# Kernel optimization log

Hardware: AMD Instinct MI355X
Metric: run time of the kernel (lower is better)

## Reference

```python
import jax, jax.numpy as jnp
import numpy as np

N = 131072   # batch of trajectory points
DX = 2       # state dim (module hardcodes Linear(2,300) in vv)
H_TM = 100   # taskmap coupling-layer hidden
H_VV = 300   # vv net hidden
H_VS = 100   # vel-scalar coupling-layer hidden


def setup_inputs() -> dict:
    key = jax.random.key(0)
    ks = iter(jax.random.split(key, 40))
    def W(i, o):
        return jax.random.normal(next(ks), (i, o), jnp.float32) / np.float32(np.sqrt(i))
    def b(o):
        return 0.01 * jax.random.normal(next(ks), (o,), jnp.float32)
    d = {"x": jax.random.normal(next(ks), (N, DX), jnp.float32)}
    # taskmap CouplingLayer nn1 (tanh MLP, residual)
    d.update(tm1_w1=W(DX, H_TM), tm1_b1=b(H_TM), tm1_w2=W(H_TM, H_TM), tm1_b2=b(H_TM), tm1_w3=W(H_TM, DX), tm1_b3=b(DX))
    # taskmap CouplingLayer nn2_1 (elu MLP -> softplus gate)
    d.update(tm2_w1=W(DX, H_TM), tm2_b1=b(H_TM), tm2_w2=W(H_TM, H_TM), tm2_b2=b(H_TM), tm2_w3=W(H_TM, DX), tm2_b3=b(DX))
    # vv net: Linear(2,300) PReLU Linear(300,300) PReLU Linear(300,2)
    d.update(vv_w1=W(DX, H_VV), vv_b1=b(H_VV), vv_a1=jnp.full((1,), 0.25, jnp.float32),
             vv_w2=W(H_VV, H_VV), vv_b2=b(H_VV), vv_a2=jnp.full((1,), 0.25, jnp.float32),
             vv_w3=W(H_VV, DX), vv_b3=b(DX))
    # log_vel_scalar CouplingLayer nn3 (leaky_relu MLP, residual via broadcast)
    d.update(vs_w1=W(DX, H_VS), vs_b1=b(H_VS), vs_w2=W(H_VS, H_VS), vs_b2=b(H_VS), vs_w3=W(H_VS, 1), vs_b3=b(1))
    return d


def reference(x, tm1_w1, tm1_b1, tm1_w2, tm1_b2, tm1_w3, tm1_b3,
              tm2_w1, tm2_b1, tm2_w2, tm2_b2, tm2_w3, tm2_b3,
              vv_w1, vv_b1, vv_a1, vv_w2, vv_b2, vv_a2, vv_w3, vv_b3,
              vs_w1, vs_b1, vs_w2, vs_b2, vs_w3, vs_b3):
    def taskmap(z):  # CouplingLayer forward with is_diffeomorphism=True; z (..., DX)
        h = jnp.tanh(z @ tm1_w1 + tm1_b1)
        h = jnp.tanh(h @ tm1_w2 + tm1_b2)
        y1 = h @ tm1_w3 + tm1_b3 + z
        g = jax.nn.elu(y1 @ tm2_w1 + tm2_b1)
        g = jax.nn.elu(g @ tm2_w2 + tm2_b2)
        s = jax.nn.softplus(g @ tm2_w3 + tm2_b3)
        return s * y1 + y1

    prelu = lambda t, a: jnp.where(t >= 0, t, a * t)
    leaky = lambda t: jnp.where(t >= 0, t, 0.01 * t)

    origin_y = taskmap(jnp.zeros((1, DX), x.dtype))        # taskmap_fcn(origin)
    y = taskmap(x) - origin_y                              # y_hat (N, DX)
    J = jax.vmap(jax.jacfwd(taskmap))(x)                   # J_hat (N, DX, DX)

    # doty_pre = vv(y_hat)
    h = prelu(y @ vv_w1 + vv_b1, vv_a1)
    h = prelu(h @ vv_w2 + vv_b2, vv_a2)
    doty = h @ vv_w3 + vv_b3                               # (N, DX)

    ls_var = jnp.sum(doty * y, axis=-1, keepdims=True)     # (N, 1)
    V_y = jnp.sum(y * y, axis=-1, keepdims=True)           # (N, 1)
    yd = doty - jax.nn.relu(ls_var + 1e-4 * V_y) * y / (V_y + 1e-12)

    J_inv = jnp.linalg.pinv(J)                             # batched pseudo-inverse
    yd_n = yd / jnp.maximum(jnp.linalg.norm(yd, axis=-1, keepdims=True), 1e-12)  # F.normalize
    xd_hat = jnp.einsum('nij,nj->ni', J_inv, yd_n)         # bmm then squeeze

    # vel_scalar = exp(log_vel_scalar(x)) + eps;  log_vel_scalar = nn3(x) + x  (broadcast (N,1)+(N,DX))
    hs = leaky(x @ vs_w1 + vs_b1)
    hs = leaky(hs @ vs_w2 + vs_b2)
    logv = (hs @ vs_w3 + vs_b3) + x                        # (N, DX) via broadcast
    xd = (jnp.exp(logv) + 1e-12) * xd_hat
    return xd
```

## Files before the change

### kernel.cpp

```cpp
#include <hip/hip_runtime.h>
#include <math.h>

#define H1 100
#define H3 300

#define WT_TM1    0
#define WT_TM2    14336
#define WT_VS     28672
#define WT_VV     43008
#define NSHORT    140288
#define F_TM1W1   0
#define F_TM1B1   256
#define F_TM2W1   384
#define F_TM2B1   640
#define F_VSW1    768
#define F_VSB1    1024
#define F_VVW1    1152
#define F_VVB1    1792
#define F_TM1B2   2112
#define F_TM2B2   2240
#define F_VSB2    2368
#define F_VVB2    2496
#define F_TM1W3T  2816
#define F_TM2W3T  3072
#define F_VSW3T   3328
#define F_VVW3T   3456
#define NFLOAT    4096

typedef __attribute__((ext_vector_type(8))) short s8v;
typedef __attribute__((ext_vector_type(4))) float f4v;

__device__ __forceinline__ f4v mfma16(s8v a, s8v b, f4v c) {
    return __builtin_amdgcn_mfma_f32_16x16x32_bf16(a, b, c, 0, 0, 0);
}
__device__ __forceinline__ float rcp_fast(float v) { return __builtin_amdgcn_rcpf(v); }
__device__ __forceinline__ float tanh_fast(float v) {
    float t = __expf(2.f * v);
    return 1.f - 2.f * rcp_fast(t + 1.f);
}
__device__ __forceinline__ float leakyf(float v) { return v >= 0.f ? v : 0.01f * v; }
__device__ __forceinline__ float preluf(float v, float a) { return v >= 0.f ? v : a * v; }
__device__ __forceinline__ short f2bf(float f) {
    union { float f; unsigned u; } v; v.f = f;
    unsigned r = v.u + 0x7fffu + ((v.u >> 16) & 1u);
    return (short)(r >> 16);
}
#define RED4(v) { v += __shfl_xor(v, 16, 64); v += __shfl_xor(v, 32, 64); }

__global__ void ngdv_prep(
    const float* __restrict__ tm1_w1, const float* __restrict__ tm1_b1,
    const float* __restrict__ tm1_w2, const float* __restrict__ tm1_b2,
    const float* __restrict__ tm1_w3, const float* __restrict__ tm1_b3,
    const float* __restrict__ tm2_w1, const float* __restrict__ tm2_b1,
    const float* __restrict__ tm2_w2, const float* __restrict__ tm2_b2,
    const float* __restrict__ tm2_w3, const float* __restrict__ tm2_b3,
    const float* __restrict__ vs_w1,  const float* __restrict__ vs_b1,
    const float* __restrict__ vs_w2,  const float* __restrict__ vs_b2,
    const float* __restrict__ vs_w3,
    const float* __restrict__ vv_w1,  const float* __restrict__ vv_b1,
    const float* __restrict__ vv_w2,  const float* __restrict__ vv_b2,
    const float* __restrict__ vv_w3,
    short* __restrict__ wsb, float* __restrict__ wsf, float* __restrict__ origin_out)
{
    const int tid = threadIdx.x;
    if (blockIdx.x < 564) {
        int idx = blockIdx.x * 256 + tid;
        if (idx < NSHORT) {
            short o;
            if (idx < WT_VV) {
                int rgn = idx / 14336, r = idx % 14336;
                const float* src = (rgn == 0) ? tm1_w2 : (rgn == 1) ? tm2_w2 : vs_w2;
                int nt = r >> 11, ks = (r >> 9) & 3, lane = (r >> 3) & 63, e = r & 7;
                int n = nt*16 + (lane & 15);
                int k = ks*32 + (lane >> 4)*8 + e;
                o = (n < H1 && k < H1) ? f2bf(src[k*H1 + n]) : (short)0;
            } else {
                int r = idx - WT_VV;
                int nt = r / 5120, rem = r % 5120;
                int ks = rem >> 9, lane = (rem >> 3) & 63, e = r & 7;
                int n = nt*16 + (lane & 15);
                int k = ks*32 + (lane >> 4)*8 + e;
                o = (n < H3 && k < H3) ? f2bf(vv_w2[k*H3 + n]) : (short)0;
            }
            wsb[idx] = o;
        } else {
            int f = idx - NSHORT;
            if (f < NFLOAT) {
                float v = 0.f;
                if (f < 256)       { int d = f >> 7, c = f & 127; if (c < H1) v = tm1_w1[d*H1 + c]; }
                else if (f < 384)  { int c = f - 256;  if (c < H1) v = tm1_b1[c]; }
                else if (f < 640)  { int r = f - 384, d = r >> 7, c = r & 127; if (c < H1) v = tm2_w1[d*H1 + c]; }
                else if (f < 768)  { int c = f - 640;  if (c < H1) v = tm2_b1[c]; }
                else if (f < 1024) { int r = f - 768, d = r >> 7, c = r & 127; if (c < H1) v = vs_w1[d*H1 + c]; }
                else if (f < 1152) { int c = f - 1024; if (c < H1) v = vs_b1[c]; }
                else if (f < 1792) { int r = f - 1152, d = r / 320, c = r % 320; if (c < H3) v = vv_w1[d*H3 + c]; }
                else if (f < 2112) { int c = f - 1792; if (c < H3) v = vv_b1[c]; }
                else if (f < 2240) { int c = f - 2112; if (c < H1) v = tm1_b2[c]; }
                else if (f < 2368) { int c = f - 2240; if (c < H1) v = tm2_b2[c]; }
                else if (f < 2496) { int c = f - 2368; if (c < H1) v = vs_b2[c]; }
                else if (f < 2816) { int c = f - 2496; if (c < H3) v = vv_b2[c]; }
                else if (f < 3072) { int r = f - 2816, i = r >> 7, c = r & 127; if (c < H1) v = tm1_w3[c*2 + i]; }
                else if (f < 3328) { int r = f - 3072, i = r >> 7, c = r & 127; if (c < H1) v = tm2_w3[c*2 + i]; }
                else if (f < 3456) { int c = f - 3328; if (c < H1) v = vs_w3[c]; }
                else               { int r = f - 3456, i = r / 320, c = r % 320; if (c < H3) v = vv_w3[c*2 + i]; }
                wsf[f] = v;
            }
        }
        return;
    }
    __shared__ float h1[H1], h2[H1], y1o[2], g1[H1], g2[H1];
    const int r = tid >> 1, hf = tid & 1;
    const int k0 = hf ? 50 : 0, k1 = hf ? 100 : 50;
    if (tid < H1) h1[tid] = tanhf(tm1_b1[tid]);
    __syncthreads();
    {
        float acc = 0.f;
        if (r < H1) for (int k = k0; k < k1; ++k) acc += h1[k] * tm1_w2[k*H1 + r];
        acc += __shfl_xor(acc, 1, 64);
        if (r < H1 && !hf) h2[r] = tanhf(acc + tm1_b2[r]);
    }
    __syncthreads();
    if (tid < 2) {
        float acc = tm1_b3[tid];
        for (int k = 0; k < H1; ++k) acc += h2[k] * tm1_w3[k*2 + tid];
        y1o[tid] = acc;
    }
    __syncthreads();
    if (tid < H1) {
        float pre = tm2_b1[tid] + y1o[0]*tm2_w1[tid] + y1o[1]*tm2_w1[H1 + tid];
        g1[tid] = pre > 0.f ? pre : expm1f(pre);
    }
    __syncthreads();
    {
        float acc = 0.f;
        if (r < H1) for (int k = k0; k < k1; ++k) acc += g1[k] * tm2_w2[k*H1 + r];
        acc += __shfl_xor(acc, 1, 64);
        if (r < H1 && !hf) { float a = acc + tm2_b2[r]; g2[r] = a > 0.f ? a : expm1f(a); }
    }
    __syncthreads();
    if (tid < 2) {
        float acc = tm2_b3[tid];
        for (int k = 0; k < H1; ++k) acc += g2[k] * tm2_w3[k*2 + tid];
        float s = acc > 20.f ? acc : log1pf(expf(acc));
        origin_out[tid] = (1.f + s) * y1o[tid];
    }
}

__global__ __launch_bounds__(512, 2) void ngdv_main(
    const float* __restrict__ x,
    const float* __restrict__ tm1_b3, const float* __restrict__ tm2_b3,
    const float* __restrict__ vs_b3,  const float* __restrict__ vv_b3,
    const float* __restrict__ vv_a1,  const float* __restrict__ vv_a2,
    const short* __restrict__ wsb,    const float* __restrict__ wsf,
    const float* __restrict__ origin, float* __restrict__ out, int npts)
{
    __shared__ __align__(16) float LW[4096];
    __shared__ __align__(16) short TMB[14336];
    __shared__ __align__(16) short VVB[2][20480];

    const int tid = threadIdx.x;
    const int wv = tid >> 6, lane = tid & 63;
    const int fm = lane & 15, fq = lane >> 4;
    const int p = blockIdx.x*128 + wv*16 + fm;
    float2 xv = {0.f, 0.f};
    if (p < npts) xv = *(const float2*)&x[p*2];
    const float og0 = origin[0], og1 = origin[1];

    for (int i = tid; i < 1024; i += 512) ((f4v*)LW)[i] = ((const f4v*)wsf)[i];
    {
        const s8v* s = (const s8v*)(wsb + WT_TM1);
        s8v* d = (s8v*)TMB;
        for (int i = tid; i < 1792; i += 512) d[i] = s[i];
    }
    __syncthreads();
    const float a1v = vv_a1[0], a2v = vv_a2[0];

    s8v afp[4], aft0[4], aft1[4];

    #pragma unroll
    for (int ks = 0; ks < 4; ++ks) {
        int c0 = ks*32 + fq*8;
        #pragma unroll
        for (int hh = 0; hh < 2; ++hh) {
            f4v w0 = *(const f4v*)&LW[F_TM1W1 + c0 + hh*4];
            f4v w1 = *(const f4v*)&LW[F_TM1W1 + 128 + c0 + hh*4];
            f4v bv = *(const f4v*)&LW[F_TM1B1 + c0 + hh*4];
            #pragma unroll
            for (int e = 0; e < 4; ++e) {
                int ee = hh*4 + e;
                float pre = fmaf(xv.y, w1[e], fmaf(xv.x, w0[e], bv[e]));
                float h = tanh_fast(pre), dd = 1.f - h*h;
                afp[ks][ee] = f2bf(h);
                aft0[ks][ee] = f2bf(w0[e]*dd);
                aft1[ks][ee] = f2bf(w1[e]*dd);
            }
        }
    }

    float y1p0 = 0.f, y1p1 = 0.f, dyp00 = 0.f, dyp01 = 0.f, dyp10 = 0.f, dyp11 = 0.f;
    #pragma unroll
    for (int nt = 0; nt < 7; ++nt) {
        s8v b0 = *(const s8v*)&TMB[(nt*4+0)*512 + lane*8];
        s8v b1 = *(const s8v*)&TMB[(nt*4+1)*512 + lane*8];
        s8v b2 = *(const s8v*)&TMB[(nt*4+2)*512 + lane*8];
        s8v b3 = *(const s8v*)&TMB[(nt*4+3)*512 + lane*8];
        f4v cp = {0,0,0,0}, ct0 = {0,0,0,0}, ct1 = {0,0,0,0};
        cp  = mfma16(b0, afp[0], cp);   cp  = mfma16(b1, afp[1], cp);
        cp  = mfma16(b2, afp[2], cp);   cp  = mfma16(b3, afp[3], cp);
        ct0 = mfma16(b0, aft0[0], ct0); ct0 = mfma16(b1, aft0[1], ct0);
        ct0 = mfma16(b2, aft0[2], ct0); ct0 = mfma16(b3, aft0[3], ct0);
        ct1 = mfma16(b0, aft1[0], ct1); ct1 = mfma16(b1, aft1[1], ct1);
        ct1 = mfma16(b2, aft1[2], ct1); ct1 = mfma16(b3, aft1[3], ct1);
        int col0 = nt*16 + fq*4;
        f4v bb2 = *(const f4v*)&LW[F_TM1B2 + col0];
        f4v w0v = *(const f4v*)&LW[F_TM1W3T + col0];
        f4v w1v = *(const f4v*)&LW[F_TM1W3T + 128 + col0];
        #pragma unroll
        for (int r = 0; r < 4; ++r) {
            float h = tanh_fast(cp[r] + bb2[r]);
            float dd = 1.f - h*h;
            float t0 = ct0[r]*dd, t1 = ct1[r]*dd;
            y1p0  = fmaf(h,  w0v[r], y1p0);  y1p1  = fmaf(h,  w1v[r], y1p1);
            dyp00 = fmaf(t0, w0v[r], dyp00); dyp01 = fmaf(t0, w1v[r], dyp01);
            dyp10 = fmaf(t1, w0v[r], dyp10); dyp11 = fmaf(t1, w1v[r], dyp11);
        }
    }
    RED4(y1p0); RED4(y1p1); RED4(dyp00); RED4(dyp01); RED4(dyp10); RED4(dyp11);
    const float y10 = y1p0 + tm1_b3[0] + xv.x;
    const float y11 = y1p1 + tm1_b3[1] + xv.y;
    const float dy00 = dyp00 + 1.f, dy01 = dyp01;
    const float dy10 = dyp10, dy11 = dyp11 + 1.f;
    __syncthreads();

    {
        const s8v* s = (const s8v*)(wsb + WT_TM2);
        s8v* d = (s8v*)TMB;
        for (int i = tid; i < 1792; i += 512) d[i] = s[i];
    }
    __syncthreads();

    #pragma unroll
    for (int ks = 0; ks < 4; ++ks) {
        int c0 = ks*32 + fq*8;
        #pragma unroll
        for (int hh = 0; hh < 2; ++hh) {
            f4v w0 = *(const f4v*)&LW[F_TM2W1 + c0 + hh*4];
            f4v w1 = *(const f4v*)&LW[F_TM2W1 + 128 + c0 + hh*4];
            f4v bv = *(const f4v*)&LW[F_TM2B1 + c0 + hh*4];
            #pragma unroll
            for (int e = 0; e < 4; ++e) {
                int ee = hh*4 + e;
                float pre = fmaf(y11, w1[e], fmaf(y10, w0[e], bv[e]));
                float g = pre > 0.f ? pre : (__expf(pre) - 1.f);
                float dd = pre > 0.f ? 1.f : (g + 1.f);
                afp[ks][ee] = f2bf(g);
                aft0[ks][ee] = f2bf((dy00*w0[e] + dy01*w1[e]) * dd);
                aft1[ks][ee] = f2bf((dy10*w0[e] + dy11*w1[e]) * dd);
            }
        }
    }

    float spp0 = 0.f, spp1 = 0.f, dsp00 = 0.f, dsp01 = 0.f, dsp10 = 0.f, dsp11 = 0.f;
    #pragma unroll
    for (int nt = 0; nt < 7; ++nt) {
        s8v b0 = *(const s8v*)&TMB[(nt*4+0)*512 + lane*8];
        s8v b1 = *(const s8v*)&TMB[(nt*4+1)*512 + lane*8];
        s8v b2 = *(const s8v*)&TMB[(nt*4+2)*512 + lane*8];
        s8v b3 = *(const s8v*)&TMB[(nt*4+3)*512 + lane*8];
        f4v cp = {0,0,0,0}, ct0 = {0,0,0,0}, ct1 = {0,0,0,0};
        cp  = mfma16(b0, afp[0], cp);   cp  = mfma16(b1, afp[1], cp);
        cp  = mfma16(b2, afp[2], cp);   cp  = mfma16(b3, afp[3], cp);
        ct0 = mfma16(b0, aft0[0], ct0); ct0 = mfma16(b1, aft0[1], ct0);
        ct0 = mfma16(b2, aft0[2], ct0); ct0 = mfma16(b3, aft0[3], ct0);
        ct1 = mfma16(b0, aft1[0], ct1); ct1 = mfma16(b1, aft1[1], ct1);
        ct1 = mfma16(b2, aft1[2], ct1); ct1 = mfma16(b3, aft1[3], ct1);
        int col0 = nt*16 + fq*4;
        f4v bb2 = *(const f4v*)&LW[F_TM2B2 + col0];
        f4v w0v = *(const f4v*)&LW[F_TM2W3T + col0];
        f4v w1v = *(const f4v*)&LW[F_TM2W3T + 128 + col0];
        #pragma unroll
        for (int r = 0; r < 4; ++r) {
            float pre = cp[r] + bb2[r];
            float g = pre > 0.f ? pre : (__expf(pre) - 1.f);
            float dd = pre > 0.f ? 1.f : (g + 1.f);
            float t0 = ct0[r]*dd, t1 = ct1[r]*dd;
            spp0  = fmaf(g,  w0v[r], spp0);  spp1  = fmaf(g,  w1v[r], spp1);
            dsp00 = fmaf(t0, w0v[r], dsp00); dsp01 = fmaf(t0, w1v[r], dsp01);
            dsp10 = fmaf(t1, w0v[r], dsp10); dsp11 = fmaf(t1, w1v[r], dsp11);
        }
    }
    RED4(spp0); RED4(spp1); RED4(dsp00); RED4(dsp01); RED4(dsp10); RED4(dsp11);
    float ys0, ys1, Ja, Jb, Jc, Jd;
    {
        float sp0 = spp0 + tm2_b3[0], sp1 = spp1 + tm2_b3[1];
        float s0 = sp0 > 20.f ? sp0 : __logf(1.f + __expf(sp0));
        float s1 = sp1 > 20.f ? sp1 : __logf(1.f + __expf(sp1));
        float sg0 = rcp_fast(1.f + __expf(-sp0));
        float sg1 = rcp_fast(1.f + __expf(-sp1));
        Ja = dsp00*sg0*y10 + (1.f + s0)*dy00;
        Jb = dsp10*sg0*y10 + (1.f + s0)*dy10;
        Jc = dsp01*sg1*y11 + (1.f + s1)*dy01;
        Jd = dsp11*sg1*y11 + (1.f + s1)*dy11;
        ys0 = (1.f + s0)*y10 - og0;
        ys1 = (1.f + s1)*y11 - og1;
    }
    __syncthreads();

    {
        const s8v* s = (const s8v*)(wsb + WT_VS);
        s8v* d = (s8v*)TMB;
        for (int i = tid; i < 1792; i += 512) d[i] = s[i];
    }
    __syncthreads();

    #pragma unroll
    for (int ks = 0; ks < 4; ++ks) {
        int c0 = ks*32 + fq*8;
        #pragma unroll
        for (int hh = 0; hh < 2; ++hh) {
            f4v w0 = *(const f4v*)&LW[F_VSW1 + c0 + hh*4];
            f4v w1 = *(const f4v*)&LW[F_VSW1 + 128 + c0 + hh*4];
            f4v bv = *(const f4v*)&LW[F_VSB1 + c0 + hh*4];
            #pragma unroll
            for (int e = 0; e < 4; ++e)
                afp[ks][hh*4+e] = f2bf(leakyf(fmaf(xv.y, w1[e], fmaf(xv.x, w0[e], bv[e]))));
        }
    }

    float lvp = 0.f;
    #pragma unroll
    for (int nt = 0; nt < 7; ++nt) {
        s8v b0 = *(const s8v*)&TMB[(nt*4+0)*512 + lane*8];
        s8v b1 = *(const s8v*)&TMB[(nt*4+1)*512 + lane*8];
        s8v b2 = *(const s8v*)&TMB[(nt*4+2)*512 + lane*8];
        s8v b3 = *(const s8v*)&TMB[(nt*4+3)*512 + lane*8];
        f4v cp = {0,0,0,0};
        cp = mfma16(b0, afp[0], cp); cp = mfma16(b1, afp[1], cp);
        cp = mfma16(b2, afp[2], cp); cp = mfma16(b3, afp[3], cp);
        int col0 = nt*16 + fq*4;
        f4v bb2 = *(const f4v*)&LW[F_VSB2 + col0];
        f4v w0v = *(const f4v*)&LW[F_VSW3T + col0];
        #pragma unroll
        for (int r = 0; r < 4; ++r)
            lvp = fmaf(leakyf(cp[r] + bb2[r]), w0v[r], lvp);
    }
    RED4(lvp);
    const float lv = lvp + vs_b3[0];

    {
        const s8v* s = (const s8v*)(wsb + WT_VV);
        s8v* d = (s8v*)VVB[0];
        for (int i = tid; i < 2560; i += 512) d[i] = s[i];
    }
    s8v afw[10];
    #pragma unroll
    for (int ks = 0; ks < 10; ++ks) {
        int c0 = ks*32 + fq*8;
        #pragma unroll
        for (int hh = 0; hh < 2; ++hh) {
            f4v w0 = *(const f4v*)&LW[F_VVW1 + c0 + hh*4];
            f4v w1 = *(const f4v*)&LW[F_VVW1 + 320 + c0 + hh*4];
            f4v bv = *(const f4v*)&LW[F_VVB1 + c0 + hh*4];
            #pragma unroll
            for (int e = 0; e < 4; ++e)
                afw[ks][hh*4+e] = f2bf(preluf(fmaf(ys1, w1[e], fmaf(ys0, w0[e], bv[e])), a1v));
        }
    }
    __syncthreads();

    float dtp0 = 0.f, dtp1 = 0.f;
    for (int c = 0; c < 5; ++c) {
        if (c < 4) {
            int n16 = (c + 1 < 4) ? 2560 : 1920;
            const s8v* s = (const s8v*)(wsb + WT_VV + (c+1)*20480);
            s8v* d = (s8v*)VVB[(c+1) & 1];
            for (int i = tid; i < n16; i += 512) d[i] = s[i];
        }
        const short* VB = VVB[c & 1];
        int ntiles = (c < 4) ? 4 : 3;
        for (int t = 0; t < ntiles; ++t) {
            int nt = c*4 + t;
            f4v cp = {0,0,0,0};
            #pragma unroll
            for (int ks = 0; ks < 10; ++ks) {
                s8v bf = *(const s8v*)&VB[(t*10 + ks)*512 + lane*8];
                cp = mfma16(bf, afw[ks], cp);
            }
            int col0 = nt*16 + fq*4;
            f4v bb2 = *(const f4v*)&LW[F_VVB2 + col0];
            f4v w0v = *(const f4v*)&LW[F_VVW3T + col0];
            f4v w1v = *(const f4v*)&LW[F_VVW3T + 320 + col0];
            #pragma unroll
            for (int r = 0; r < 4; ++r) {
                float v = preluf(cp[r] + bb2[r], a2v);
                dtp0 = fmaf(v, w0v[r], dtp0);
                dtp1 = fmaf(v, w1v[r], dtp1);
            }
        }
        __syncthreads();
    }
    RED4(dtp0); RED4(dtp1);
    const float dt0 = dtp0 + vv_b3[0];
    const float dt1 = dtp1 + vv_b3[1];

    if (fq == 0 && p < npts) {
        float ls = dt0*ys0 + dt1*ys1;
        float Vq = ys0*ys0 + ys1*ys1;
        float coef = fmaxf(ls + 1e-4f*Vq, 0.f) * rcp_fast(Vq + 1e-12f);
        float yd0 = dt0 - coef*ys0, yd1 = dt1 - coef*ys1;
        float inv_n = rcp_fast(fmaxf(sqrtf(yd0*yd0 + yd1*yd1), 1e-12f));
        float yn0 = yd0*inv_n, yn1 = yd1*inv_n;
        float invdet = rcp_fast(Ja*Jd - Jb*Jc);
        float xh0 = ( Jd*yn0 - Jb*yn1) * invdet;
        float xh1 = (-Jc*yn0 + Ja*yn1) * invdet;
        float2 o;
        o.x = (__expf(lv + xv.x) + 1e-12f) * xh0;
        o.y = (__expf(lv + xv.y) + 1e-12f) * xh1;
        *(float2*)&out[p*2] = o;
    }
}

extern "C" void kernel_launch(void* const* d_in, const int* in_sizes, int n_in,
                              void* d_out, int out_size, void* d_ws, size_t ws_size,
                              hipStream_t stream) {
    const float* x      = (const float*)d_in[0];
    const float* tm1_w1 = (const float*)d_in[1];
    const float* tm1_b1 = (const float*)d_in[2];
    const float* tm1_w2 = (const float*)d_in[3];
    const float* tm1_b2 = (const float*)d_in[4];
    const float* tm1_w3 = (const float*)d_in[5];
    const float* tm1_b3 = (const float*)d_in[6];
    const float* tm2_w1 = (const float*)d_in[7];
    const float* tm2_b1 = (const float*)d_in[8];
    const float* tm2_w2 = (const float*)d_in[9];
    const float* tm2_b2 = (const float*)d_in[10];
    const float* tm2_w3 = (const float*)d_in[11];
    const float* tm2_b3 = (const float*)d_in[12];
    const float* vv_w1  = (const float*)d_in[13];
    const float* vv_b1  = (const float*)d_in[14];
    const float* vv_a1  = (const float*)d_in[15];
    const float* vv_w2  = (const float*)d_in[16];
    const float* vv_b2  = (const float*)d_in[17];
    const float* vv_a2  = (const float*)d_in[18];
    const float* vv_w3  = (const float*)d_in[19];
    const float* vv_b3  = (const float*)d_in[20];
    const float* vs_w1  = (const float*)d_in[21];
    const float* vs_b1  = (const float*)d_in[22];
    const float* vs_w2  = (const float*)d_in[23];
    const float* vs_b2  = (const float*)d_in[24];
    const float* vs_w3  = (const float*)d_in[25];
    const float* vs_b3  = (const float*)d_in[26];

    float* out       = (float*)d_out;
    float* origin_ws = (float*)d_ws;
    short* wsb       = (short*)((char*)d_ws + 64);
    float* wsf       = (float*)((char*)d_ws + 64 + NSHORT*2);
    const int npts = in_sizes[0] / 2;
    const int nblk = (npts + 127) / 128;

    ngdv_prep<<<565, 256, 0, stream>>>(
        tm1_w1, tm1_b1, tm1_w2, tm1_b2, tm1_w3, tm1_b3,
        tm2_w1, tm2_b1, tm2_w2, tm2_b2, tm2_w3, tm2_b3,
        vs_w1, vs_b1, vs_w2, vs_b2, vs_w3,
        vv_w1, vv_b1, vv_w2, vv_b2, vv_w3,
        wsb, wsf, origin_ws);

    ngdv_main<<<nblk, 512, 0, stream>>>(
        x, tm1_b3, tm2_b3, vs_b3, vv_b3, vv_a1, vv_a2,
        wsb, wsf, origin_ws, out, npts);
}
```

Before: 245.6 us.

## Shrink LDS footprint with per-tile VV streaming and raise occupancy target

Drops the separate TM and double-buffered 4-tile VV shared buffers and reuses one 28 KB buffer for every stage. The VV layer-2 weights now stream one 16-column tile at a time, double-buffered, with a barrier per tile. Launch bounds go from 2 to 4 blocks per CU so more blocks can be resident. The origin kernel's 100-term output dot products become wave-parallel shuffle reductions instead of 2-thread serial loops. The trade is 19 barriers instead of 5 in the VV loop, with less work between barriers to hide the global loads, and a tighter register budget that may cause spills.

```diff
diff --git a/kernel.cpp b/kernel.cpp
--- a/kernel.cpp
+++ b/kernel.cpp
@@ -120,10 +120,14 @@
         if (r < H1 && !hf) h2[r] = tanhf(acc + tm1_b2[r]);
     }
     __syncthreads();
-    if (tid < 2) {
-        float acc = tm1_b3[tid];
-        for (int k = 0; k < H1; ++k) acc += h2[k] * tm1_w3[k*2 + tid];
-        y1o[tid] = acc;
+    if (tid < 128) {
+        int i = tid >> 6, ln = tid & 63;
+        float acc = 0.f;
+        if (ln < H1) acc += h2[ln] * tm1_w3[ln*2 + i];
+        if (ln + 64 < H1) acc += h2[ln+64] * tm1_w3[(ln+64)*2 + i];
+        #pragma unroll
+        for (int off = 32; off >= 1; off >>= 1) acc += __shfl_xor(acc, off, 64);
+        if (ln == 0) y1o[i] = acc + tm1_b3[i];
     }
     __syncthreads();
     if (tid < H1) {
@@ -138,15 +142,22 @@
         if (r < H1 && !hf) { float a = acc + tm2_b2[r]; g2[r] = a > 0.f ? a : expm1f(a); }
     }
     __syncthreads();
-    if (tid < 2) {
-        float acc = tm2_b3[tid];
-        for (int k = 0; k < H1; ++k) acc += g2[k] * tm2_w3[k*2 + tid];
-        float s = acc > 20.f ? acc : log1pf(expf(acc));
-        origin_out[tid] = (1.f + s) * y1o[tid];
-    }
-}
-
-__global__ __launch_bounds__(512, 2) void ngdv_main(
+    if (tid < 128) {
+        int i = tid >> 6, ln = tid & 63;
+        float acc = 0.f;
+        if (ln < H1) acc += g2[ln] * tm2_w3[ln*2 + i];
+        if (ln + 64 < H1) acc += g2[ln+64] * tm2_w3[(ln+64)*2 + i];
+        #pragma unroll
+        for (int off = 32; off >= 1; off >>= 1) acc += __shfl_xor(acc, off, 64);
+        if (ln == 0) {
+            float a = acc + tm2_b3[i];
+            float s = a > 20.f ? a : log1pf(expf(a));
+            origin_out[i] = (1.f + s) * y1o[i];
+        }
+    }
+}
+
+__global__ __launch_bounds__(512, 4) void ngdv_main(
     const float* __restrict__ x,
     const float* __restrict__ tm1_b3, const float* __restrict__ tm2_b3,
     const float* __restrict__ vs_b3,  const float* __restrict__ vv_b3,
@@ -155,8 +166,7 @@
     const float* __restrict__ origin, float* __restrict__ out, int npts)
 {
     __shared__ __align__(16) float LW[4096];
-    __shared__ __align__(16) short TMB[14336];
-    __shared__ __align__(16) short VVB[2][20480];
+    __shared__ __align__(16) short WB[14336];
 
     const int tid = threadIdx.x;
     const int wv = tid >> 6, lane = tid & 63;
@@ -169,7 +179,7 @@
     for (int i = tid; i < 1024; i += 512) ((f4v*)LW)[i] = ((const f4v*)wsf)[i];
     {
         const s8v* s = (const s8v*)(wsb + WT_TM1);
-        s8v* d = (s8v*)TMB;
+        s8v* d = (s8v*)WB;
         for (int i = tid; i < 1792; i += 512) d[i] = s[i];
     }
     __syncthreads();
@@ -200,10 +210,10 @@
     float y1p0 = 0.f, y1p1 = 0.f, dyp00 = 0.f, dyp01 = 0.f, dyp10 = 0.f, dyp11 = 0.f;
     #pragma unroll
     for (int nt = 0; nt < 7; ++nt) {
-        s8v b0 = *(const s8v*)&TMB[(nt*4+0)*512 + lane*8];
-        s8v b1 = *(const s8v*)&TMB[(nt*4+1)*512 + lane*8];
-        s8v b2 = *(const s8v*)&TMB[(nt*4+2)*512 + lane*8];
-        s8v b3 = *(const s8v*)&TMB[(nt*4+3)*512 + lane*8];
+        s8v b0 = *(const s8v*)&WB[(nt*4+0)*512 + lane*8];
+        s8v b1 = *(const s8v*)&WB[(nt*4+1)*512 + lane*8];
+        s8v b2 = *(const s8v*)&WB[(nt*4+2)*512 + lane*8];
+        s8v b3 = *(const s8v*)&WB[(nt*4+3)*512 + lane*8];
         f4v cp = {0,0,0,0}, ct0 = {0,0,0,0}, ct1 = {0,0,0,0};
         cp  = mfma16(b0, afp[0], cp);   cp  = mfma16(b1, afp[1], cp);
         cp  = mfma16(b2, afp[2], cp);   cp  = mfma16(b3, afp[3], cp);
@@ -234,7 +244,7 @@
 
     {
         const s8v* s = (const s8v*)(wsb + WT_TM2);
-        s8v* d = (s8v*)TMB;
+        s8v* d = (s8v*)WB;
         for (int i = tid; i < 1792; i += 512) d[i] = s[i];
     }
     __syncthreads();
@@ -263,10 +273,10 @@
     float spp0 = 0.f, spp1 = 0.f, dsp00 = 0.f, dsp01 = 0.f, dsp10 = 0.f, dsp11 = 0.f;
     #pragma unroll
     for (int nt = 0; nt < 7; ++nt) {
-        s8v b0 = *(const s8v*)&TMB[(nt*4+0)*512 + lane*8];
-        s8v b1 = *(const s8v*)&TMB[(nt*4+1)*512 + lane*8];
-        s8v b2 = *(const s8v*)&TMB[(nt*4+2)*512 + lane*8];
-        s8v b3 = *(const s8v*)&TMB[(nt*4+3)*512 + lane*8];
+        s8v b0 = *(const s8v*)&WB[(nt*4+0)*512 + lane*8];
+        s8v b1 = *(const s8v*)&WB[(nt*4+1)*512 + lane*8];
+        s8v b2 = *(const s8v*)&WB[(nt*4+2)*512 + lane*8];
+        s8v b3 = *(const s8v*)&WB[(nt*4+3)*512 + lane*8];
         f4v cp = {0,0,0,0}, ct0 = {0,0,0,0}, ct1 = {0,0,0,0};
         cp  = mfma16(b0, afp[0], cp);   cp  = mfma16(b1, afp[1], cp);
         cp  = mfma16(b2, afp[2], cp);   cp  = mfma16(b3, afp[3], cp);
@@ -308,7 +318,7 @@
 
     {
         const s8v* s = (const s8v*)(wsb + WT_VS);
-        s8v* d = (s8v*)TMB;
+        s8v* d = (s8v*)WB;
         for (int i = tid; i < 1792; i += 512) d[i] = s[i];
     }
     __syncthreads();
@@ -330,10 +340,10 @@
     float lvp = 0.f;
     #pragma unroll
     for (int nt = 0; nt < 7; ++nt) {
-        s8v b0 = *(const s8v*)&TMB[(nt*4+0)*512 + lane*8];
-        s8v b1 = *(const s8v*)&TMB[(nt*4+1)*512 + lane*8];
-        s8v b2 = *(const s8v*)&TMB[(nt*4+2)*512 + lane*8];
-        s8v b3 = *(const s8v*)&TMB[(nt*4+3)*512 + lane*8];
+        s8v b0 = *(const s8v*)&WB[(nt*4+0)*512 + lane*8];
+        s8v b1 = *(const s8v*)&WB[(nt*4+1)*512 + lane*8];
+        s8v b2 = *(const s8v*)&WB[(nt*4+2)*512 + lane*8];
+        s8v b3 = *(const s8v*)&WB[(nt*4+3)*512 + lane*8];
         f4v cp = {0,0,0,0};
         cp = mfma16(b0, afp[0], cp); cp = mfma16(b1, afp[1], cp);
         cp = mfma16(b2, afp[2], cp); cp = mfma16(b3, afp[3], cp);
@@ -346,11 +356,12 @@
     }
     RED4(lvp);
     const float lv = lvp + vs_b3[0];
+    __syncthreads();
 
     {
         const s8v* s = (const s8v*)(wsb + WT_VV);
-        s8v* d = (s8v*)VVB[0];
-        for (int i = tid; i < 2560; i += 512) d[i] = s[i];
+        s8v* d = (s8v*)WB;
+        for (int i = tid; i < 640; i += 512) d[i] = s[i];
     }
     s8v afw[10];
     #pragma unroll
@@ -369,33 +380,28 @@
     __syncthreads();
 
     float dtp0 = 0.f, dtp1 = 0.f;
-    for (int c = 0; c < 5; ++c) {
-        if (c < 4) {
-            int n16 = (c + 1 < 4) ? 2560 : 1920;
-            const s8v* s = (const s8v*)(wsb + WT_VV + (c+1)*20480);
-            s8v* d = (s8v*)VVB[(c+1) & 1];
-            for (int i = tid; i < n16; i += 512) d[i] = s[i];
-        }
-        const short* VB = VVB[c & 1];
-        int ntiles = (c < 4) ? 4 : 3;
-        for (int t = 0; t < ntiles; ++t) {
-            int nt = c*4 + t;
-            f4v cp = {0,0,0,0};
-            #pragma unroll
-            for (int ks = 0; ks < 10; ++ks) {
-                s8v bf = *(const s8v*)&VB[(t*10 + ks)*512 + lane*8];
-                cp = mfma16(bf, afw[ks], cp);
-            }
-            int col0 = nt*16 + fq*4;
-            f4v bb2 = *(const f4v*)&LW[F_VVB2 + col0];
-            f4v w0v = *(const f4v*)&LW[F_VVW3T + col0];
-            f4v w1v = *(const f4v*)&LW[F_VVW3T + 320 + col0];
-            #pragma unroll
-            for (int r = 0; r < 4; ++r) {
-                float v = preluf(cp[r] + bb2[r], a2v);
-                dtp0 = fmaf(v, w0v[r], dtp0);
-                dtp1 = fmaf(v, w1v[r], dtp1);
-            }
+    for (int t = 0; t < 19; ++t) {
+        if (t < 18) {
+            const s8v* s = (const s8v*)(wsb + WT_VV + (t+1)*5120);
+            s8v* d = (s8v*)(WB + ((t+1) & 1)*5120);
+            for (int i = tid; i < 640; i += 512) d[i] = s[i];
+        }
+        const short* VB = WB + (t & 1)*5120;
+        f4v cp = {0,0,0,0};
+        #pragma unroll
+        for (int ks = 0; ks < 10; ++ks) {
+            s8v bf = *(const s8v*)&VB[ks*512 + lane*8];
+            cp = mfma16(bf, afw[ks], cp);
+        }
+        int col0 = t*16 + fq*4;
+        f4v bb2 = *(const f4v*)&LW[F_VVB2 + col0];
+        f4v w0v = *(const f4v*)&LW[F_VVW3T + col0];
+        f4v w1v = *(const f4v*)&LW[F_VVW3T + 320 + col0];
+        #pragma unroll
+        for (int r = 0; r < 4; ++r) {
+            float v = preluf(cp[r] + bb2[r], a2v);
+            dtp0 = fmaf(v, w0v[r], dtp0);
+            dtp1 = fmaf(v, w1v[r], dtp1);
         }
         __syncthreads();
     }
```

After: 234.7 us. 4.4% less time.
